# Optimization experiments

Measured on AMD Instinct MI355X. Metric: run time of the kernel, lower is better.

The kernel has to match this reference:

```python
import jax, jax.numpy as jnp
import numpy as np

N_NODES = 100000


def _mean_agg(x, src, dst, n_nodes):
    # gather neighbor (src) features, segment-sum into destination nodes, divide by in-degree
    summed = jax.ops.segment_sum(x[src], dst, num_segments=n_nodes)  # [N, d]
    deg = jax.ops.segment_sum(jnp.ones_like(dst, dtype=x.dtype), dst, num_segments=n_nodes)
    return summed / jnp.clip(deg, 1.0)[:, None]  # DGL clamps zero in-degree to 1


def _sage_conv(x, src, dst, W_self, W_neigh, b, n_nodes):
    h_neigh = _mean_agg(x, src, dst, n_nodes)
    # DGL SAGEConv(mean): fc_self(h_self) + fc_neigh(h_neigh); single bias
    return x @ W_self + h_neigh @ W_neigh + b


def setup_inputs() -> dict:
    key = jax.random.key(0)
    ks = jax.random.split(key, 8)
    in_f, hid_f, out_f = 64, 64, 16
    n_edges = 1200000
    return {
        "x": jax.random.normal(ks[0], (N_NODES, in_f), dtype=jnp.float32),
        "src": jax.random.randint(ks[1], (n_edges,), 0, N_NODES),
        "dst": jax.random.randint(ks[2], (n_edges,), 0, N_NODES),
        "W1_self": jax.random.normal(ks[3], (in_f, hid_f), dtype=jnp.float32) / np.sqrt(in_f),
        "W1_neigh": jax.random.normal(ks[4], (in_f, hid_f), dtype=jnp.float32) / np.sqrt(in_f),
        "b1": jnp.zeros((hid_f,), dtype=jnp.float32),
        "W2_self": jax.random.normal(ks[5], (hid_f, out_f), dtype=jnp.float32) / np.sqrt(hid_f),
        "W2_neigh": jax.random.normal(ks[6], (hid_f, out_f), dtype=jnp.float32) / np.sqrt(hid_f),
        "b2": jnp.zeros((out_f,), dtype=jnp.float32),
    }


def reference(x, src, dst, W1_self, W1_neigh, b1, W2_self, W2_neigh, b2):
    h = _sage_conv(x, src, dst, W1_self, W1_neigh, b1, N_NODES)
    h = jax.nn.relu(h)
    h = _sage_conv(h, src, dst, W2_self, W2_neigh, b2, N_NODES)
    return h
```

## Files before the change

### kernel.cpp

```cpp
#include <hip/hip_runtime.h>

#define N_NODES 100000
#define N_EDGES 1200000
#define BK 128
#define NB 782
#define CHUNK_E 4096
#define NBLK_E 293
#define TOT_H (NB * NBLK_E)
#define NSB2 ((TOT_H + 1023) / 1024)
#define CAP 4096

#define OFF_ROWPTR 0
#define OFF_HISTG  400896
#define OFF_HSCAN  1317632
#define OFF_BLK2   2234368
#define OFF_PAIRS  2235392
#define OFF_SORTED 7035392
#define OFF_Y1     11835392
#define OFF_H1     24635392

__device__ __forceinline__ unsigned short f2bf(float f) {
    unsigned u = __float_as_uint(f);
    unsigned r = (u + 0x7fffu + ((u >> 16) & 1u)) >> 16;
    return (unsigned short)r;
}


__global__ __launch_bounds__(256) void chunk_hist_kernel(
    const int* __restrict__ dst, int* __restrict__ hist_g)
{
    __shared__ int h[NB];
    const int e0 = blockIdx.x * CHUNK_E;
    const int e1 = min(e0 + CHUNK_E, N_EDGES);
    for (int i = threadIdx.x; i < NB; i += 256) h[i] = 0;
    __syncthreads();
    for (int e = e0 + threadIdx.x; e < e1; e += 256)
        atomicAdd(&h[dst[e] >> 7], 1);
    __syncthreads();
    for (int i = threadIdx.x; i < NB; i += 256)
        hist_g[i * NBLK_E + blockIdx.x] = h[i];
}

__global__ __launch_bounds__(1024) void scan2_blocks_kernel(
    const int* __restrict__ hist_g, int* __restrict__ hs_scan, int* __restrict__ blk2)
{
    __shared__ int s[1024];
    int i = blockIdx.x * 1024 + threadIdx.x;
    int v = (i < TOT_H) ? hist_g[i] : 0;
    s[threadIdx.x] = v;
    __syncthreads();
    for (int off = 1; off < 1024; off <<= 1) {
        int t = (threadIdx.x >= off) ? s[threadIdx.x - off] : 0;
        __syncthreads();
        s[threadIdx.x] += t;
        __syncthreads();
    }
    if (i < TOT_H) hs_scan[i] = s[threadIdx.x] - v;
    if (threadIdx.x == 1023) blk2[blockIdx.x] = s[1023];
}

__global__ __launch_bounds__(256) void scan2_tops_kernel(int* __restrict__ blk2)
{
    __shared__ int s[256];
    int v = (threadIdx.x < NSB2) ? blk2[threadIdx.x] : 0;
    s[threadIdx.x] = v;
    __syncthreads();
    for (int off = 1; off < 256; off <<= 1) {
        int t = (threadIdx.x >= off) ? s[threadIdx.x - off] : 0;
        __syncthreads();
        s[threadIdx.x] += t;
        __syncthreads();
    }
    if (threadIdx.x < NSB2) blk2[threadIdx.x] = s[threadIdx.x] - v;
}

__global__ __launch_bounds__(256) void pair_scatter_kernel(
    const int* __restrict__ src, const int* __restrict__ dst,
    const int* __restrict__ hs_scan, const int* __restrict__ blk2,
    unsigned* __restrict__ pairs)
{
    __shared__ int base_s[NB];
    __shared__ int cur_s[NB];
    const int b = blockIdx.x;
    const int e0 = b * CHUNK_E;
    const int e1 = min(e0 + CHUNK_E, N_EDGES);

    for (int i = threadIdx.x; i < NB; i += 256) {
        int idx = i * NBLK_E + b;
        base_s[i] = hs_scan[idx] + blk2[idx >> 10];
        cur_s[i] = 0;
    }
    __syncthreads();
    for (int e = e0 + threadIdx.x; e < e1; e += 256) {
        int d = dst[e];
        int bk = d >> 7;
        int pos = base_s[bk] + atomicAdd(&cur_s[bk], 1);
        pairs[pos] = ((unsigned)src[e] << 7) | (unsigned)(d & 127);
    }
}


__global__ __launch_bounds__(256) void dense1_kernel(
    const float* __restrict__ x,
    const float* __restrict__ Wn, const float* __restrict__ Ws,
    const float* __restrict__ b,
    unsigned short* __restrict__ y1, float* __restrict__ z1)
{
    __shared__ float sx[32 * 64];
    const int t = threadIdx.x;
    const int w = t >> 6;
    const int lane = t & 63;
    const int half = w >> 1;
    const int nsub = (w & 1) * 16;
    const int chunk = blockIdx.x * 32;

    {
        const float4* gx = (const float4*)(x + (size_t)chunk * 64);
        float4* sx4 = (float4*)sx;
        sx4[t] = gx[t];
        sx4[t + 256] = gx[t + 256];
    }

    const float* W = half ? Ws : Wn;
    float wr[64];
#pragma unroll
    for (int k = 0; k < 64; ++k) wr[k] = W[k * 64 + lane];
    const float bj = half ? b[lane] : 0.f;

    __syncthreads();

#pragma unroll 1
    for (int m = 0; m < 16; ++m) {
        const int node = nsub + m;
        const float4* xr = (const float4*)(sx + node * 64);
        float a0 = 0.f, a1 = 0.f, a2 = 0.f, a3 = 0.f;
#pragma unroll
        for (int k4 = 0; k4 < 16; ++k4) {
            float4 v = xr[k4];
            a0 += v.x * wr[4 * k4 + 0];
            a1 += v.y * wr[4 * k4 + 1];
            a2 += v.z * wr[4 * k4 + 2];
            a3 += v.w * wr[4 * k4 + 3];
        }
        const float o = (a0 + a1) + (a2 + a3) + bj;
        const size_t gn = (size_t)(chunk + node);
        if (half) z1[gn * 64 + lane] = o;
        else      y1[gn * 64 + lane] = f2bf(o);
    }
}

__global__ __launch_bounds__(256) void dense2_kernel(
    const float* __restrict__ h1,
    const float* __restrict__ Wn, const float* __restrict__ Ws,
    const float* __restrict__ b,
    float* __restrict__ y2, float* __restrict__ out)
{
    __shared__ float sx[32 * 68];
    const int t = threadIdx.x;
    const int w = t >> 6;
    const int lane = t & 63;
    const int half = w >> 1;
    const int nsub = (w & 1) * 16;
    const int j = lane & 15;
    const int g = lane >> 4;
    const int chunk = blockIdx.x * 32;

    {
        const float4* gx = (const float4*)(h1 + (size_t)chunk * 64);
        float4* sx4 = (float4*)sx;
        int r0 = t >> 4, c0 = t & 15;
        sx4[r0 * 17 + c0] = gx[t];
        sx4[(r0 + 16) * 17 + c0] = gx[t + 256];
    }

    const float* W = half ? Ws : Wn;
    float wr[64];
#pragma unroll
    for (int k = 0; k < 64; ++k) wr[k] = W[k * 16 + j];
    const float bj = half ? b[j] : 0.f;

    __syncthreads();

#pragma unroll 1
    for (int q = 0; q < 4; ++q) {
        const int node = nsub + q * 4 + g;
        const float4* xr = (const float4*)(sx + node * 68);
        float a0 = 0.f, a1 = 0.f, a2 = 0.f, a3 = 0.f;
#pragma unroll
        for (int k4 = 0; k4 < 16; ++k4) {
            float4 v = xr[k4];
            a0 += v.x * wr[4 * k4 + 0];
            a1 += v.y * wr[4 * k4 + 1];
            a2 += v.z * wr[4 * k4 + 2];
            a3 += v.w * wr[4 * k4 + 3];
        }
        const float o = (a0 + a1) + (a2 + a3) + bj;
        const size_t gn = (size_t)(chunk + node);
        if (half) out[gn * 16 + j] = o;
        else      y2[gn * 16 + j] = o;
    }
}

__global__ __launch_bounds__(512) void fused_gather1_kernel(
    const unsigned short* __restrict__ y1,
    const unsigned* __restrict__ pairs,
    const int* __restrict__ hs_scan, const int* __restrict__ blk2,
    int* __restrict__ row_ptr, int* __restrict__ sorted_src,
    float* __restrict__ h1)
{
    __shared__ int slist[CAP];
    __shared__ int hist[BK];
    __shared__ int sc[BK];
    __shared__ int cur[BK];
    const int b = blockIdx.x;
    const int t = threadIdx.x;
    const int lane = t & 63;
    const int wv = t >> 6;
    const int g = lane >> 3;
    const int fl = lane & 7;

    const int i0 = b * NBLK_E;
    const int start = hs_scan[i0] + blk2[i0 >> 10];
    const int end = (b == NB - 1) ? N_EDGES
                    : hs_scan[i0 + NBLK_E] + blk2[(i0 + NBLK_E) >> 10];
    const int cnt = end - start;
    const int node0 = b * BK;

    if (t < BK) hist[t] = 0;
    __syncthreads();
    for (int e = start + t; e < end; e += 512)
        atomicAdd(&hist[pairs[e] & 127u], 1);
    __syncthreads();

    int v = (t < BK) ? hist[t] : 0;
    if (t < BK) sc[t] = v;
    __syncthreads();
    for (int off = 1; off < BK; off <<= 1) {
        int tv = (t >= off && t < BK) ? sc[t - off] : 0;
        __syncthreads();
        if (t < BK) sc[t] += tv;
        __syncthreads();
    }
    const int excl = (t < BK) ? sc[t] - v : 0;
    if (t < BK && node0 + t < N_NODES) row_ptr[node0 + t] = start + excl;
    if (b == NB - 1 && t == 0) row_ptr[N_NODES] = N_EDGES;
    if (t < BK) cur[t] = excl;
    __syncthreads();

    if (cnt <= CAP) {
        for (int e = start + t; e < end; e += 512) {
            unsigned u = pairs[e];
            int p = atomicAdd(&cur[u & 127u], 1);
            slist[p] = (int)(u >> 7);
        }
        __syncthreads();
        for (int i = t; i < cnt; i += 512)
            sorted_src[start + i] = slist[i];
        for (int m = 0; m < 16; ++m) {
            const int node = wv * 16 + m;
            const int gn = node0 + node;
            if (gn >= N_NODES) break;
            const int o = sc[node] - hist[node];
            const int dg = hist[node];
            float a0 = 0.f, a1 = 0.f, a2 = 0.f, a3 = 0.f;
            float a4 = 0.f, a5 = 0.f, a6 = 0.f, a7 = 0.f;
            for (int base = 0; base < dg; base += 8) {
                const int idx = base + g;
                if (idx < dg) {
                    const int s = slist[o + idx];
                    uint4 raw = ((const uint4*)(y1 + (size_t)s * 64))[fl];
                    a0 += __uint_as_float(raw.x << 16);
                    a1 += __uint_as_float(raw.x & 0xffff0000u);
                    a2 += __uint_as_float(raw.y << 16);
                    a3 += __uint_as_float(raw.y & 0xffff0000u);
                    a4 += __uint_as_float(raw.z << 16);
                    a5 += __uint_as_float(raw.z & 0xffff0000u);
                    a6 += __uint_as_float(raw.w << 16);
                    a7 += __uint_as_float(raw.w & 0xffff0000u);
                }
            }
#pragma unroll
            for (int d = 8; d <= 32; d <<= 1) {
                a0 += __shfl_xor(a0, d); a1 += __shfl_xor(a1, d);
                a2 += __shfl_xor(a2, d); a3 += __shfl_xor(a3, d);
                a4 += __shfl_xor(a4, d); a5 += __shfl_xor(a5, d);
                a6 += __shfl_xor(a6, d); a7 += __shfl_xor(a7, d);
            }
            const float invd = 1.0f / (float)max(dg, 1);
            if (g == 0) {
                float4* hp = (float4*)(h1 + (size_t)gn * 64);
                float4 z0 = hp[fl * 2];
                float4 z1v = hp[fl * 2 + 1];
                hp[fl * 2] = make_float4(fmaxf(z0.x + a0 * invd, 0.f),
                                         fmaxf(z0.y + a1 * invd, 0.f),
                                         fmaxf(z0.z + a2 * invd, 0.f),
                                         fmaxf(z0.w + a3 * invd, 0.f));
                hp[fl * 2 + 1] = make_float4(fmaxf(z1v.x + a4 * invd, 0.f),
                                             fmaxf(z1v.y + a5 * invd, 0.f),
                                             fmaxf(z1v.z + a6 * invd, 0.f),
                                             fmaxf(z1v.w + a7 * invd, 0.f));
            }
        }
    } else {
        if (t < BK) cur[t] = start + excl;
        __syncthreads();
        for (int e = start + t; e < end; e += 512) {
            unsigned u = pairs[e];
            int p = atomicAdd(&cur[u & 127u], 1);
            sorted_src[p] = (int)(u >> 7);
        }
        __syncthreads();
        for (int m = 0; m < 16; ++m) {
            const int node = wv * 16 + m;
            const int gn = node0 + node;
            if (gn >= N_NODES) break;
            const int o = start + sc[node] - hist[node];
            const int dg = hist[node];
            float a0 = 0.f, a1 = 0.f, a2 = 0.f, a3 = 0.f;
            float a4 = 0.f, a5 = 0.f, a6 = 0.f, a7 = 0.f;
            for (int base = 0; base < dg; base += 8) {
                const int idx = base + g;
                if (idx < dg) {
                    const int s = sorted_src[o + idx];
                    uint4 raw = ((const uint4*)(y1 + (size_t)s * 64))[fl];
                    a0 += __uint_as_float(raw.x << 16);
                    a1 += __uint_as_float(raw.x & 0xffff0000u);
                    a2 += __uint_as_float(raw.y << 16);
                    a3 += __uint_as_float(raw.y & 0xffff0000u);
                    a4 += __uint_as_float(raw.z << 16);
                    a5 += __uint_as_float(raw.z & 0xffff0000u);
                    a6 += __uint_as_float(raw.w << 16);
                    a7 += __uint_as_float(raw.w & 0xffff0000u);
                }
            }
#pragma unroll
            for (int d = 8; d <= 32; d <<= 1) {
                a0 += __shfl_xor(a0, d); a1 += __shfl_xor(a1, d);
                a2 += __shfl_xor(a2, d); a3 += __shfl_xor(a3, d);
                a4 += __shfl_xor(a4, d); a5 += __shfl_xor(a5, d);
                a6 += __shfl_xor(a6, d); a7 += __shfl_xor(a7, d);
            }
            const float invd = 1.0f / (float)max(dg, 1);
            if (g == 0) {
                float4* hp = (float4*)(h1 + (size_t)gn * 64);
                float4 z0 = hp[fl * 2];
                float4 z1v = hp[fl * 2 + 1];
                hp[fl * 2] = make_float4(fmaxf(z0.x + a0 * invd, 0.f),
                                         fmaxf(z0.y + a1 * invd, 0.f),
                                         fmaxf(z0.z + a2 * invd, 0.f),
                                         fmaxf(z0.w + a3 * invd, 0.f));
                hp[fl * 2 + 1] = make_float4(fmaxf(z1v.x + a4 * invd, 0.f),
                                             fmaxf(z1v.y + a5 * invd, 0.f),
                                             fmaxf(z1v.z + a6 * invd, 0.f),
                                             fmaxf(z1v.w + a7 * invd, 0.f));
            }
        }
    }
}

__global__ __launch_bounds__(256) void gather2_kernel(
    const float* __restrict__ y2,
    const int* __restrict__ row_ptr,
    const int* __restrict__ sorted_src,
    float* __restrict__ out)
{
    const int w = threadIdx.x >> 6;
    const int lane = threadIdx.x & 63;
    const int n = blockIdx.x * 4 + w;
    const int group = lane >> 2;
    const int fl = lane & 3;

    const int start = row_ptr[n];
    const int deg = row_ptr[n + 1] - start;

    float4 acc = make_float4(0.f, 0.f, 0.f, 0.f);
    for (int base = 0; base < deg; base += 64) {
        const int m = min(64, deg - base);
        int eid = 0;
        if (lane < m) eid = sorted_src[start + base + lane];
        for (int jj = 0; jj < m; jj += 16) {
            const int idx = jj + group;
            const int s = __shfl(eid, idx);
            if (idx < m) {
                float4 v = ((const float4*)(y2 + (size_t)s * 16))[fl];
                acc.x += v.x; acc.y += v.y; acc.z += v.z; acc.w += v.w;
            }
        }
    }
#pragma unroll
    for (int d = 4; d <= 32; d <<= 1) {
        acc.x += __shfl_xor(acc.x, d); acc.y += __shfl_xor(acc.y, d);
        acc.z += __shfl_xor(acc.z, d); acc.w += __shfl_xor(acc.w, d);
    }
    const float invd = 1.0f / (float)max(deg, 1);
    if (lane < 4) {
        float4* op = (float4*)(out + (size_t)n * 16);
        float4 z = op[fl];
        op[fl] = make_float4(z.x + acc.x * invd, z.y + acc.y * invd,
                             z.z + acc.z * invd, z.w + acc.w * invd);
    }
}

extern "C" void kernel_launch(void* const* d_in, const int* in_sizes, int n_in,
                              void* d_out, int out_size, void* d_ws, size_t ws_size,
                              hipStream_t stream) {
    const float* x   = (const float*)d_in[0];
    const int*   src = (const int*)d_in[1];
    const int*   dst = (const int*)d_in[2];
    const float* W1s = (const float*)d_in[3];
    const float* W1n = (const float*)d_in[4];
    const float* b1  = (const float*)d_in[5];
    const float* W2s = (const float*)d_in[6];
    const float* W2n = (const float*)d_in[7];
    const float* b2  = (const float*)d_in[8];
    float* out = (float*)d_out;

    char* ws = (char*)d_ws;
    int* row_ptr    = (int*)(ws + OFF_ROWPTR);
    int* hist_g     = (int*)(ws + OFF_HISTG);
    int* hs_scan    = (int*)(ws + OFF_HSCAN);
    int* blk2       = (int*)(ws + OFF_BLK2);
    unsigned* pairs = (unsigned*)(ws + OFF_PAIRS);
    int* sorted_src = (int*)(ws + OFF_SORTED);
    unsigned short* y1 = (unsigned short*)(ws + OFF_Y1);
    float* y2       = (float*)(ws + OFF_Y1);
    float* h1       = (float*)(ws + OFF_H1);

    chunk_hist_kernel<<<NBLK_E, 256, 0, stream>>>(dst, hist_g);
    scan2_blocks_kernel<<<NSB2, 1024, 0, stream>>>(hist_g, hs_scan, blk2);
    scan2_tops_kernel<<<1, 256, 0, stream>>>(blk2);
    pair_scatter_kernel<<<NBLK_E, 256, 0, stream>>>(src, dst, hs_scan, blk2, pairs);

    dense1_kernel<<<3125, 256, 0, stream>>>(x, W1n, W1s, b1, y1, h1);
    fused_gather1_kernel<<<NB, 512, 0, stream>>>(y1, pairs, hs_scan, blk2,
                                                 row_ptr, sorted_src, h1);

    dense2_kernel<<<3125, 256, 0, stream>>>(h1, W2n, W2s, b2, y2, out);
    gather2_kernel<<<N_NODES / 4, 256, 0, stream>>>(y2, row_ptr, sorted_src, out);
}
```

Measured before the change: 247.4 us.

## Merge histogram into dense1 launch and fold top-level scan into consumers

Combines the edge-chunk histogram and the first dense transform into one launch, with block-index ranges selecting which job each block runs, so the two independent stages overlap. Removes the single-block top-level scan kernel; each pair_scatter and fused_gather1 block now redoes the 256-entry scan of blk2 in shared memory. This cuts two kernel launches and their serialization gaps, at the cost of redundant per-block scan work and extra barriers in the consumer kernels.

```diff
diff --git a/kernel.cpp b/kernel.cpp
--- a/kernel.cpp
+++ b/kernel.cpp
@@ -9,6 +9,7 @@
 #define TOT_H (NB * NBLK_E)
 #define NSB2 ((TOT_H + 1023) / 1024)
 #define CAP 4096
+#define ND1 3125
 
 #define OFF_ROWPTR 0
 #define OFF_HISTG  400896
@@ -25,82 +26,8 @@
     return (unsigned short)r;
 }
 
-
-__global__ __launch_bounds__(256) void chunk_hist_kernel(
-    const int* __restrict__ dst, int* __restrict__ hist_g)
-{
-    __shared__ int h[NB];
-    const int e0 = blockIdx.x * CHUNK_E;
-    const int e1 = min(e0 + CHUNK_E, N_EDGES);
-    for (int i = threadIdx.x; i < NB; i += 256) h[i] = 0;
-    __syncthreads();
-    for (int e = e0 + threadIdx.x; e < e1; e += 256)
-        atomicAdd(&h[dst[e] >> 7], 1);
-    __syncthreads();
-    for (int i = threadIdx.x; i < NB; i += 256)
-        hist_g[i * NBLK_E + blockIdx.x] = h[i];
-}
-
-__global__ __launch_bounds__(1024) void scan2_blocks_kernel(
-    const int* __restrict__ hist_g, int* __restrict__ hs_scan, int* __restrict__ blk2)
-{
-    __shared__ int s[1024];
-    int i = blockIdx.x * 1024 + threadIdx.x;
-    int v = (i < TOT_H) ? hist_g[i] : 0;
-    s[threadIdx.x] = v;
-    __syncthreads();
-    for (int off = 1; off < 1024; off <<= 1) {
-        int t = (threadIdx.x >= off) ? s[threadIdx.x - off] : 0;
-        __syncthreads();
-        s[threadIdx.x] += t;
-        __syncthreads();
-    }
-    if (i < TOT_H) hs_scan[i] = s[threadIdx.x] - v;
-    if (threadIdx.x == 1023) blk2[blockIdx.x] = s[1023];
-}
-
-__global__ __launch_bounds__(256) void scan2_tops_kernel(int* __restrict__ blk2)
-{
-    __shared__ int s[256];
-    int v = (threadIdx.x < NSB2) ? blk2[threadIdx.x] : 0;
-    s[threadIdx.x] = v;
-    __syncthreads();
-    for (int off = 1; off < 256; off <<= 1) {
-        int t = (threadIdx.x >= off) ? s[threadIdx.x - off] : 0;
-        __syncthreads();
-        s[threadIdx.x] += t;
-        __syncthreads();
-    }
-    if (threadIdx.x < NSB2) blk2[threadIdx.x] = s[threadIdx.x] - v;
-}
-
-__global__ __launch_bounds__(256) void pair_scatter_kernel(
-    const int* __restrict__ src, const int* __restrict__ dst,
-    const int* __restrict__ hs_scan, const int* __restrict__ blk2,
-    unsigned* __restrict__ pairs)
-{
-    __shared__ int base_s[NB];
-    __shared__ int cur_s[NB];
-    const int b = blockIdx.x;
-    const int e0 = b * CHUNK_E;
-    const int e1 = min(e0 + CHUNK_E, N_EDGES);
-
-    for (int i = threadIdx.x; i < NB; i += 256) {
-        int idx = i * NBLK_E + b;
-        base_s[i] = hs_scan[idx] + blk2[idx >> 10];
-        cur_s[i] = 0;
-    }
-    __syncthreads();
-    for (int e = e0 + threadIdx.x; e < e1; e += 256) {
-        int d = dst[e];
-        int bk = d >> 7;
-        int pos = base_s[bk] + atomicAdd(&cur_s[bk], 1);
-        pairs[pos] = ((unsigned)src[e] << 7) | (unsigned)(d & 127);
-    }
-}
-
-
-__global__ __launch_bounds__(256) void dense1_kernel(
+__global__ __launch_bounds__(256) void hist_dense1_kernel(
+    const int* __restrict__ dst, int* __restrict__ hist_g,
     const float* __restrict__ x,
     const float* __restrict__ Wn, const float* __restrict__ Ws,
     const float* __restrict__ b,
@@ -108,11 +35,27 @@
 {
     __shared__ float sx[32 * 64];
     const int t = threadIdx.x;
+
+    if (blockIdx.x < NBLK_E) {
+        int* h = (int*)sx;
+        const int e0 = blockIdx.x * CHUNK_E;
+        const int e1 = min(e0 + CHUNK_E, N_EDGES);
+        for (int i = t; i < NB; i += 256) h[i] = 0;
+        __syncthreads();
+        for (int e = e0 + t; e < e1; e += 256)
+            atomicAdd(&h[dst[e] >> 7], 1);
+        __syncthreads();
+        for (int i = t; i < NB; i += 256)
+            hist_g[i * NBLK_E + blockIdx.x] = h[i];
+        return;
+    }
+
+    const int bid = blockIdx.x - NBLK_E;
     const int w = t >> 6;
     const int lane = t & 63;
     const int half = w >> 1;
     const int nsub = (w & 1) * 16;
-    const int chunk = blockIdx.x * 32;
+    const int chunk = bid * 32;
 
     {
         const float4* gx = (const float4*)(x + (size_t)chunk * 64);
@@ -149,55 +92,70 @@
     }
 }
 
-__global__ __launch_bounds__(256) void dense2_kernel(
-    const float* __restrict__ h1,
-    const float* __restrict__ Wn, const float* __restrict__ Ws,
-    const float* __restrict__ b,
-    float* __restrict__ y2, float* __restrict__ out)
-{
-    __shared__ float sx[32 * 68];
+__global__ __launch_bounds__(1024) void scan2_blocks_kernel(
+    const int* __restrict__ hist_g, int* __restrict__ hs_scan, int* __restrict__ blk2)
+{
+    __shared__ int s[1024];
+    int i = blockIdx.x * 1024 + threadIdx.x;
+    int v = (i < TOT_H) ? hist_g[i] : 0;
+    s[threadIdx.x] = v;
+    __syncthreads();
+    for (int off = 1; off < 1024; off <<= 1) {
+        int t = (threadIdx.x >= off) ? s[threadIdx.x - off] : 0;
+        __syncthreads();
+        s[threadIdx.x] += t;
+        __syncthreads();
+    }
+    if (i < TOT_H) hs_scan[i] = s[threadIdx.x] - v;
+    if (threadIdx.x == 1023) blk2[blockIdx.x] = s[1023];
+}
+
+__device__ __forceinline__ void local_tops_scan(const int* blk2, int* tops, int t)
+{
+    if (t < 256) {
+        int v = (t < NSB2) ? blk2[t] : 0;
+        tops[t] = v;
+    }
+    __syncthreads();
+    for (int off = 1; off < 256; off <<= 1) {
+        int tv = (t >= off && t < 256) ? tops[t - off] : 0;
+        __syncthreads();
+        if (t < 256) tops[t] += tv;
+        __syncthreads();
+    }
+    int ex = 0;
+    if (t < 256) ex = tops[t] - ((t < NSB2) ? blk2[t] : 0);
+    __syncthreads();
+    if (t < 256) tops[t] = ex;
+    __syncthreads();
+}
+
+__global__ __launch_bounds__(256) void pair_scatter_kernel(
+    const int* __restrict__ src, const int* __restrict__ dst,
+    const int* __restrict__ hs_scan, const int* __restrict__ blk2,
+    unsigned* __restrict__ pairs)
+{
+    __shared__ int base_s[NB];
+    __shared__ int cur_s[NB];
+    __shared__ int tops[256];
+    const int b = blockIdx.x;
     const int t = threadIdx.x;
-    const int w = t >> 6;
-    const int lane = t & 63;
-    const int half = w >> 1;
-    const int nsub = (w & 1) * 16;
-    const int j = lane & 15;
-    const int g = lane >> 4;
-    const int chunk = blockIdx.x * 32;
-
-    {
-        const float4* gx = (const float4*)(h1 + (size_t)chunk * 64);
-        float4* sx4 = (float4*)sx;
-        int r0 = t >> 4, c0 = t & 15;
-        sx4[r0 * 17 + c0] = gx[t];
-        sx4[(r0 + 16) * 17 + c0] = gx[t + 256];
-    }
-
-    const float* W = half ? Ws : Wn;
-    float wr[64];
-#pragma unroll
-    for (int k = 0; k < 64; ++k) wr[k] = W[k * 16 + j];
-    const float bj = half ? b[j] : 0.f;
-
-    __syncthreads();
-
-#pragma unroll 1
-    for (int q = 0; q < 4; ++q) {
-        const int node = nsub + q * 4 + g;
-        const float4* xr = (const float4*)(sx + node * 68);
-        float a0 = 0.f, a1 = 0.f, a2 = 0.f, a3 = 0.f;
-#pragma unroll
-        for (int k4 = 0; k4 < 16; ++k4) {
-            float4 v = xr[k4];
-            a0 += v.x * wr[4 * k4 + 0];
-            a1 += v.y * wr[4 * k4 + 1];
-            a2 += v.z * wr[4 * k4 + 2];
-            a3 += v.w * wr[4 * k4 + 3];
-        }
-        const float o = (a0 + a1) + (a2 + a3) + bj;
-        const size_t gn = (size_t)(chunk + node);
-        if (half) out[gn * 16 + j] = o;
-        else      y2[gn * 16 + j] = o;
+    const int e0 = b * CHUNK_E;
+    const int e1 = min(e0 + CHUNK_E, N_EDGES);
+
+    local_tops_scan(blk2, tops, t);
+
+    for (int i = t; i < NB; i += 256) {
+        int idx = i * NBLK_E + b;
+        base_s[i] = hs_scan[idx] + tops[idx >> 10];
+        cur_s[i] = 0;
+    }
+    __syncthreads();
+    for (int e = e0 + t; e < e1; e += 256) {
+        int d = dst[e];
+        int bk = d >> 7;
+        int pos = base_s[bk] + atomicAdd(&cur_s[bk], 1);
+        pairs[pos] = ((unsigned)src[e] << 7) | (unsigned)(d & 127);
     }
 }
 
@@ -212,6 +170,7 @@
     __shared__ int hist[BK];
     __shared__ int sc[BK];
     __shared__ int cur[BK];
+    __shared__ int tops[256];
     const int b = blockIdx.x;
     const int t = threadIdx.x;
     const int lane = t & 63;
@@ -219,10 +178,12 @@
     const int g = lane >> 3;
     const int fl = lane & 7;
 
+    local_tops_scan(blk2, tops, t);
+
     const int i0 = b * NBLK_E;
-    const int start = hs_scan[i0] + blk2[i0 >> 10];
+    const int start = hs_scan[i0] + tops[i0 >> 10];
     const int end = (b == NB - 1) ? N_EDGES
-                    : hs_scan[i0 + NBLK_E] + blk2[(i0 + NBLK_E) >> 10];
+                    : hs_scan[i0 + NBLK_E] + tops[(i0 + NBLK_E) >> 10];
     const int cnt = end - start;
     const int node0 = b * BK;
 
@@ -358,6 +319,58 @@
     }
 }
 
+__global__ __launch_bounds__(256) void dense2_kernel(
+    const float* __restrict__ h1,
+    const float* __restrict__ Wn, const float* __restrict__ Ws,
+    const float* __restrict__ b,
+    float* __restrict__ y2, float* __restrict__ out)
+{
+    __shared__ float sx[32 * 68];
+    const int t = threadIdx.x;
+    const int w = t >> 6;
+    const int lane = t & 63;
+    const int half = w >> 1;
+    const int nsub = (w & 1) * 16;
+    const int j = lane & 15;
+    const int g = lane >> 4;
+    const int chunk = blockIdx.x * 32;
+
+    {
+        const float4* gx = (const float4*)(h1 + (size_t)chunk * 64);
+        float4* sx4 = (float4*)sx;
+        int r0 = t >> 4, c0 = t & 15;
+        sx4[r0 * 17 + c0] = gx[t];
+        sx4[(r0 + 16) * 17 + c0] = gx[t + 256];
+    }
+
+    const float* W = half ? Ws : Wn;
+    float wr[64];
+#pragma unroll
+    for (int k = 0; k < 64; ++k) wr[k] = W[k * 16 + j];
+    const float bj = half ? b[j] : 0.f;
+
+    __syncthreads();
+
+#pragma unroll 1
+    for (int q = 0; q < 4; ++q) {
+        const int node = nsub + q * 4 + g;
+        const float4* xr = (const float4*)(sx + node * 68);
+        float a0 = 0.f, a1 = 0.f, a2 = 0.f, a3 = 0.f;
+#pragma unroll
+        for (int k4 = 0; k4 < 16; ++k4) {
+            float4 v = xr[k4];
+            a0 += v.x * wr[4 * k4 + 0];
+            a1 += v.y * wr[4 * k4 + 1];
+            a2 += v.z * wr[4 * k4 + 2];
+            a3 += v.w * wr[4 * k4 + 3];
+        }
+        const float o = (a0 + a1) + (a2 + a3) + bj;
+        const size_t gn = (size_t)(chunk + node);
+        if (half) out[gn * 16 + j] = o;
+        else      y2[gn * 16 + j] = o;
+    }
+}
+
 __global__ __launch_bounds__(256) void gather2_kernel(
     const float* __restrict__ y2,
     const int* __restrict__ row_ptr,
@@ -426,15 +439,12 @@
     float* y2       = (float*)(ws + OFF_Y1);
     float* h1       = (float*)(ws + OFF_H1);
 
-    chunk_hist_kernel<<<NBLK_E, 256, 0, stream>>>(dst, hist_g);
+    hist_dense1_kernel<<<NBLK_E + ND1, 256, 0, stream>>>(
+        dst, hist_g, x, W1n, W1s, b1, y1, h1);
     scan2_blocks_kernel<<<NSB2, 1024, 0, stream>>>(hist_g, hs_scan, blk2);
-    scan2_tops_kernel<<<1, 256, 0, stream>>>(blk2);
     pair_scatter_kernel<<<NBLK_E, 256, 0, stream>>>(src, dst, hs_scan, blk2, pairs);
-
-    dense1_kernel<<<3125, 256, 0, stream>>>(x, W1n, W1s, b1, y1, h1);
     fused_gather1_kernel<<<NB, 512, 0, stream>>>(y1, pairs, hs_scan, blk2,
                                                  row_ptr, sorted_src, h1);
-
-    dense2_kernel<<<3125, 256, 0, stream>>>(h1, W2n, W2s, b2, y2, out);
+    dense2_kernel<<<ND1, 256, 0, stream>>>(h1, W2n, W2s, b2, y2, out);
     gather2_kernel<<<N_NODES / 4, 256, 0, stream>>>(y2, row_ptr, sorted_src, out);
 }
```

New measurement: 240.9 us. -2.6%, faster.
